# Optimization experiments

Measured on AMD Instinct MI355X. Metric: run time of the kernel, lower is better.

Reference implementation:

```python
import jax, jax.numpy as jnp
import numpy as np

E = 1024   # embed_dim
H = 16     # num_heads
D = E // H # head_dim
B = 2
S = 2048
YAT_EPS = 0.1


def setup_inputs() -> dict:
    key = jax.random.key(0)
    ks = jax.random.split(key, 5)
    w_scale = (6.0 / (E + E)) ** 0.5  # xavier_uniform bound
    def xavier(k):
        return jax.random.uniform(k, (E, E), jnp.float32, -w_scale, w_scale)
    return {
        "x": jax.random.normal(ks[0], (B, S, E), jnp.float32),
        "Wq": xavier(ks[1]), "bq": jnp.zeros((E,), jnp.float32),
        "Wk": xavier(ks[2]), "bk": jnp.zeros((E,), jnp.float32),
        "Wv": xavier(ks[3]), "bv": jnp.zeros((E,), jnp.float32),
        "Wo": xavier(ks[4]), "bo": jnp.zeros((E,), jnp.float32),
    }


def reference(x, Wq, bq, Wk, bk, Wv, bv, Wo, bo):
    b, s, _ = x.shape
    # Projections (Linear: x @ W + b, flax kernel layout [in, out])
    Q = x @ Wq + bq
    K = x @ Wk + bk
    V = x @ Wv + bv
    # [B, H, S, D]
    Q = Q.reshape(b, s, H, D).transpose(0, 2, 1, 3)
    K = K.reshape(b, s, H, D).transpose(0, 2, 1, 3)
    V = V.reshape(b, s, H, D).transpose(0, 2, 1, 3)
    # L2 normalize along head_dim
    Qn = Q / (jnp.linalg.norm(Q, axis=-1, keepdims=True) + 1e-8)
    Kn = K / (jnp.linalg.norm(K, axis=-1, keepdims=True) + 1e-8)
    # Yat kernel scores: (1 + <q,k>)^2 / (eps + (1 - <q,k>))
    dot = jnp.einsum("bhqd,bhkd->bhqk", Qn, Kn)
    scores = (1.0 + dot) ** 2 / (YAT_EPS + (1.0 - dot))
    # Sum-normalize (no softmax)
    attn = scores / (jnp.sum(scores, axis=-1, keepdims=True) + 1e-6)
    out = jnp.einsum("bhqk,bhkd->bhqd", attn, V)
    out = out.transpose(0, 2, 1, 3).reshape(b, s, E)
    return out @ Wo + bo
```

## Files before the change

kernel.cpp:

```cpp
#include <hip/hip_runtime.h>
#include <math.h>

#define EDIM 1024
#define NH   16
#define HD   64
#define BATCH 2
#define SEQ  2048
#define NROW (BATCH*SEQ)
#define YAT_EPS 0.1f

typedef _Float16 f16;
typedef _Float16 f16x8 __attribute__((ext_vector_type(8)));
typedef _Float16 f16x4 __attribute__((ext_vector_type(4)));
typedef __fp16   h16x2 __attribute__((ext_vector_type(2)));
typedef float    f32x4 __attribute__((ext_vector_type(4)));

static __device__ __forceinline__ int pk2(float a, float b) {
    union { h16x2 h; int i; } u;
    u.h = __builtin_amdgcn_cvt_pkrtz(a, b);
    return u.i;
}

__global__ __launch_bounds__(256)
void prep_kernel(const float* __restrict__ x, f16* __restrict__ xb,
                 const float* __restrict__ W0, const float* __restrict__ W1,
                 const float* __restrict__ W2, const float* __restrict__ W3,
                 f16* __restrict__ T0, f16* __restrict__ T1,
                 f16* __restrict__ T2, f16* __restrict__ T3)
{
    const int z = blockIdx.z;
    if (z == 4) {
        const int bid = blockIdx.y * 32 + blockIdx.x;
#pragma unroll
        for (int i = 0; i < 4; ++i) {
            const int off = bid * 4096 + i * 1024 + threadIdx.x * 4;
            const float4 v = *(const float4*)(x + off);
            union { int i2[2]; f16x4 h; } o;
            o.i2[0] = pk2(v.x, v.y);
            o.i2[1] = pk2(v.z, v.w);
            *(f16x4*)(xb + off) = o.h;
        }
        return;
    }
    const float* W = (z == 0) ? W0 : (z == 1) ? W1 : (z == 2) ? W2 : W3;
    f16*         Wt = (z == 0) ? T0 : (z == 1) ? T1 : (z == 2) ? T2 : T3;

    __shared__ float T[32][33];
    const int t = threadIdx.x;
    const int r = t >> 3, c4 = (t & 7) * 4;
    const int bi = blockIdx.x * 32, bj = blockIdx.y * 32;
    const float4 v = *(const float4*)(W + (size_t)(bi + r) * 1024 + bj + c4);
    T[r][c4 + 0] = v.x; T[r][c4 + 1] = v.y; T[r][c4 + 2] = v.z; T[r][c4 + 3] = v.w;
    __syncthreads();
    f16x4 o = {(f16)T[c4 + 0][r], (f16)T[c4 + 1][r], (f16)T[c4 + 2][r], (f16)T[c4 + 3][r]};
    *(f16x4*)(Wt + (size_t)(bj + r) * 1024 + bi + c4) = o;
}

template<int BM, int BN, int WM>
__global__ __launch_bounds__(WM * 128, 3)
void gemm_f16(const f16* __restrict__ A,
              const f16* __restrict__ B0, const f16* __restrict__ B1, const f16* __restrict__ B2,
              const float* __restrict__ bi0, const float* __restrict__ bi1, const float* __restrict__ bi2,
              void* __restrict__ o0, void* __restrict__ o1, void* __restrict__ o2,
              int e0, int e1, int e2)
{
    constexpr int NT    = WM * 128;
    constexpr int SR    = NT / 4;
    constexpr int ASL   = BM / SR;
    constexpr int BSL   = BN / SR;
    constexpr int ABUF  = BM * 32;
    constexpr int BBUF  = BN * 32;
    constexpr int WROWS = BM / WM;
    constexpr int MT    = WROWS / 16;
    constexpr int HALVES = BN / 128;
    constexpr int SCH    = 2048 / NT;
    __shared__ __align__(16) char lds[2 * (ABUF + BBUF) * 2];
    f16* As = (f16*)lds;
    f16* Bs = (f16*)lds + 2 * ABUF;

    const int z = blockIdx.z;
    const f16*   Bt   = (z == 0) ? B0  : (z == 1) ? B1  : B2;
    const float* bias = (z == 0) ? bi0 : (z == 1) ? bi1 : bi2;
    void*        Cout = (z == 0) ? o0  : (z == 1) ? o1  : o2;
    const int    epi  = (z == 0) ? e0  : (z == 1) ? e1  : e2;

    const int tid  = threadIdx.x;
    const int lane = tid & 63;
    const int w    = tid >> 6;
    const int cl   = lane & 15;
    const int quad = lane >> 4;
    const int wm = w % WM, wn = w / WM;
    const int bm = blockIdx.x * BM, bn = blockIdx.y * BN;
    const int wmoff = wm * WROWS;

    const int srow = tid >> 2;
    const int sc   = tid & 3;
    const int ssw  = (sc ^ (srow & 3)) * 8;
    const f16* gA = A  + (size_t)(bm + srow) * 1024 + sc * 8;
    const f16* gB = Bt + (size_t)(bn + srow) * 1024 + sc * 8;
    int lAo[ASL], lBo[BSL];
#pragma unroll
    for (int i = 0; i < ASL; ++i) lAo[i] = (srow + i * SR) * 32 + ssw;
#pragma unroll
    for (int i = 0; i < BSL; ++i) lBo[i] = (srow + i * SR) * 32 + ssw;

    f32x4 acc[MT][4];
#pragma unroll
    for (int i = 0; i < MT; ++i)
#pragma unroll
        for (int j = 0; j < 4; ++j) acc[i][j] = (f32x4){0.f, 0.f, 0.f, 0.f};

    f16x8 ra[ASL], rb[BSL];

#pragma unroll
    for (int i = 0; i < ASL; ++i) ra[i] = *(const f16x8*)(gA + (size_t)i * SR * 1024);
#pragma unroll
    for (int i = 0; i < BSL; ++i) rb[i] = *(const f16x8*)(gB + (size_t)i * SR * 1024);
#pragma unroll
    for (int i = 0; i < ASL; ++i) *(f16x8*)(As + lAo[i]) = ra[i];
#pragma unroll
    for (int i = 0; i < BSL; ++i) *(f16x8*)(Bs + lBo[i]) = rb[i];
#pragma unroll
    for (int i = 0; i < ASL; ++i) ra[i] = *(const f16x8*)(gA + (size_t)i * SR * 1024 + 32);
#pragma unroll
    for (int i = 0; i < BSL; ++i) rb[i] = *(const f16x8*)(gB + (size_t)i * SR * 1024 + 32);
    __syncthreads();

    const int fsw = (quad ^ (cl & 3)) * 8;

    for (int it = 0; it < 32; ++it) {
        const int buf = it & 1, nb = buf ^ 1;
        if (it < 31) {
#pragma unroll
            for (int i = 0; i < ASL; ++i) *(f16x8*)(As + nb * ABUF + lAo[i]) = ra[i];
#pragma unroll
            for (int i = 0; i < BSL; ++i) *(f16x8*)(Bs + nb * BBUF + lBo[i]) = rb[i];
        }
        if (it < 30) {
            const int kn = (it + 2) * 32;
#pragma unroll
            for (int i = 0; i < ASL; ++i) ra[i] = *(const f16x8*)(gA + (size_t)i * SR * 1024 + kn);
#pragma unroll
            for (int i = 0; i < BSL; ++i) rb[i] = *(const f16x8*)(gB + (size_t)i * SR * 1024 + kn);
        }
        f16x8 af[MT], bf[4];
#pragma unroll
        for (int mt = 0; mt < MT; ++mt)
            af[mt] = *(const f16x8*)(&As[buf * ABUF + (wmoff + mt * 16 + cl) * 32 + fsw]);
#pragma unroll
        for (int nt = 0; nt < 4; ++nt)
            bf[nt] = *(const f16x8*)(&Bs[buf * BBUF + (wn * 64 + nt * 16 + cl) * 32 + fsw]);
#pragma unroll
        for (int mt = 0; mt < MT; ++mt)
#pragma unroll
            for (int nt = 0; nt < 4; ++nt)
                acc[mt][nt] = __builtin_amdgcn_mfma_f32_16x16x32_f16(af[mt], bf[nt], acc[mt][nt], 0, 0, 0);
        __syncthreads();
    }

    float bcol[4];
#pragma unroll
    for (int nt = 0; nt < 4; ++nt) bcol[nt] = bias[bn + wn * 64 + nt * 16 + cl];
#pragma unroll
    for (int mt = 0; mt < MT; ++mt)
#pragma unroll
        for (int nt = 0; nt < 4; ++nt)
#pragma unroll
            for (int rg = 0; rg < 4; ++rg) acc[mt][nt][rg] += bcol[nt];

    const int b_idx = bm >> 11, sl0 = bm & (SEQ - 1), h0 = bn >> 6;

    if (epi == 0) {
        float* C = (float*)Cout;
#pragma unroll
        for (int mt = 0; mt < MT; ++mt)
#pragma unroll
            for (int rg = 0; rg < 4; ++rg) {
                const int row = bm + wmoff + mt * 16 + quad * 4 + rg;
#pragma unroll
                for (int nt = 0; nt < 4; ++nt)
                    C[(size_t)row * EDIM + bn + wn * 64 + nt * 16 + cl] = acc[mt][nt][rg];
            }
    } else if (epi == 1) {
        if constexpr (BM == 128) {
        f16* C = (f16*)Cout;
        f16* S = (f16*)lds;
#pragma unroll
        for (int h = 0; h < HALVES; ++h) {
            __syncthreads();
            if ((wn >> 1) == h) {
#pragma unroll
                for (int mt = 0; mt < MT; ++mt)
#pragma unroll
                    for (int rg = 0; rg < 4; ++rg) {
                        float ss = 0.f;
#pragma unroll
                        for (int nt = 0; nt < 4; ++nt) ss += acc[mt][nt][rg] * acc[mt][nt][rg];
                        ss += __shfl_xor(ss, 1); ss += __shfl_xor(ss, 2);
                        ss += __shfl_xor(ss, 4); ss += __shfl_xor(ss, 8);
                        const float inv = 1.0f / (sqrtf(ss) + 1e-8f);
                        const int row = wmoff + mt * 16 + quad * 4 + rg;
#pragma unroll
                        for (int nt = 0; nt < 4; ++nt) {
                            const int colh = (wn & 1) * 64 + nt * 16 + cl;
                            S[row * 128 + (((colh >> 3) ^ (row & 15)) * 8) + (colh & 7)] =
                                (f16)(acc[mt][nt][rg] * inv);
                        }
                    }
            }
            __syncthreads();
#pragma unroll
            for (int i = 0; i < SCH; ++i) {
                const int c = tid + i * NT;
                const int s = c >> 4, gi = c & 15;
                f16x8 v = *(const f16x8*)(&S[s * 128 + ((gi ^ (s & 15)) * 8)]);
                const int head = h0 + h * 2 + (gi >> 3), d8 = (gi & 7) * 8;
                *(f16x8*)(C + ((size_t)(b_idx * NH + head) * SEQ + sl0 + s) * HD + d8) = v;
            }
        }
        }
    } else {
        if constexpr (BM == 128) {
        f16* C = (f16*)Cout;
        f16* S = (f16*)lds;
#pragma unroll
        for (int h = 0; h < HALVES; ++h) {
            __syncthreads();
            if ((wn >> 1) == h) {
#pragma unroll
                for (int mt = 0; mt < MT; ++mt) {
                    const int s0 = wmoff + mt * 16 + quad * 4;
#pragma unroll
                    for (int nt = 0; nt < 4; ++nt) {
                        const int colh = (wn & 1) * 64 + nt * 16 + cl;
                        f16x4 o = {(f16)acc[mt][nt][0], (f16)acc[mt][nt][1],
                                   (f16)acc[mt][nt][2], (f16)acc[mt][nt][3]};
                        *(f16x4*)(&S[colh * 128 + (((s0 >> 3) ^ (colh & 15)) * 8) + (s0 & 7)]) = o;
                    }
                }
            }
            __syncthreads();
#pragma unroll
            for (int i = 0; i < SCH; ++i) {
                const int c = tid + i * NT;
                const int colh = c >> 4, gi = c & 15;
                f16x8 v = *(const f16x8*)(&S[colh * 128 + ((gi ^ (colh & 15)) * 8)]);
                const int head = h0 + h * 2 + (colh >> 6), d = colh & 63;
                *(f16x8*)(C + ((size_t)(b_idx * NH + head) * HD + d) * SEQ + sl0 + gi * 8) = v;
            }
        }
        }
    }
}

__global__ __launch_bounds__(256, 4)
void yat_attn(const f16* __restrict__ Qh, const f16* __restrict__ Kh,
              const f16* __restrict__ Vt, f16* __restrict__ AO)
{
    __shared__ __align__(16) char lds[40960];
    f16* Qs = (f16*)lds;
    f16* KB = (f16*)(lds + 8192);
    f16* VB = (f16*)(lds + 24576);

    const int tid  = threadIdx.x;
    const int lane = tid & 63;
    const int w    = tid >> 6;
    const int cl   = lane & 15;
    const int quad = lane >> 4;
    const int wm = w & 1;
    const int wk = w >> 1;
    const int q0 = blockIdx.x * 64;
    const int bh = blockIdx.y;

    const f16* Qg = Qh + (size_t)bh * SEQ * HD;
    const f16* Kg = Kh + (size_t)bh * SEQ * HD;
    const f16* Vg = Vt + (size_t)bh * HD * SEQ;

    const int r0 = tid >> 3;
    const int g0 = tid & 7;
    const f16* gK = Kg + (size_t)r0 * HD + g0 * 8;
    const f16* gV = Vg + (size_t)r0 * SEQ + g0 * 8;
    const int lkOff = r0 * 64 + ((g0 ^ (r0 & 7)) * 8);

    f16x8 kr0 = *(const f16x8*)(gK);
    f16x8 kr1 = *(const f16x8*)(gK + 32 * HD);
    f16x8 vr0 = *(const f16x8*)(gV);
    f16x8 vr1 = *(const f16x8*)(gV + (size_t)32 * SEQ);

#pragma unroll
    for (int i = 0; i < 2; ++i) {
        const int s0 = tid + i * 256;
        const int row = s0 >> 3, g = s0 & 7;
        f16x8 v = *(const f16x8*)(Qg + (size_t)(q0 + row) * HD + g * 8);
        *(f16x8*)(&Qs[row * 64 + ((g ^ (row & 7)) * 8)]) = v;
    }
    __syncthreads();
    f16x8 qf[2][2];
#pragma unroll
    for (int qt = 0; qt < 2; ++qt)
#pragma unroll
        for (int kb = 0; kb < 2; ++kb)
            qf[qt][kb] = *(const f16x8*)(&Qs[(wm * 32 + qt * 16 + cl) * 64 +
                                             ((kb * 4 + quad) ^ (cl & 7)) * 8]);

    f32x4 O[2][4];
    float rs[2] = {0.f, 0.f};
#pragma unroll
    for (int i = 0; i < 2; ++i)
#pragma unroll
        for (int j = 0; j < 4; ++j) O[i][j] = (f32x4){0.f, 0.f, 0.f, 0.f};

    for (int t = 0; t < 32; ++t) {
        const int buf = t & 1;
        *(f16x8*)(&KB[buf * 4096 + lkOff])        = kr0;
        *(f16x8*)(&KB[buf * 4096 + lkOff + 2048]) = kr1;
        *(f16x8*)(&VB[buf * 4096 + lkOff])        = vr0;
        *(f16x8*)(&VB[buf * 4096 + lkOff + 2048]) = vr1;
        if (t < 31) {
            kr0 = *(const f16x8*)(gK + (size_t)(t + 1) * 64 * HD);
            kr1 = *(const f16x8*)(gK + (size_t)(t + 1) * 64 * HD + 32 * HD);
            vr0 = *(const f16x8*)(gV + (t + 1) * 64);
            vr1 = *(const f16x8*)(gV + (size_t)32 * SEQ + (t + 1) * 64);
        }
        __syncthreads();

        const f16* Ks = KB + buf * 4096;
        const f16* Vs = VB + buf * 4096;

        f32x4 s[2][2];
#pragma unroll
        for (int kt = 0; kt < 2; ++kt)
#pragma unroll
            for (int qt = 0; qt < 2; ++qt) s[kt][qt] = (f32x4){0.f, 0.f, 0.f, 0.f};
#pragma unroll
        for (int kb = 0; kb < 2; ++kb) {
            const int sw = ((kb * 4 + quad) ^ (cl & 7)) * 8;
            f16x8 af0 = *(const f16x8*)(&Ks[(wk * 32 +  0 + cl) * 64 + sw]);
            f16x8 af1 = *(const f16x8*)(&Ks[(wk * 32 + 16 + cl) * 64 + sw]);
#pragma unroll
            for (int qt = 0; qt < 2; ++qt) {
                s[0][qt] = __builtin_amdgcn_mfma_f32_16x16x32_f16(af0, qf[qt][kb], s[0][qt], 0, 0, 0);
                s[1][qt] = __builtin_amdgcn_mfma_f32_16x16x32_f16(af1, qf[qt][kb], s[1][qt], 0, 0, 0);
            }
        }

        f16x4 pa16[2][2];
#pragma unroll
        for (int kt = 0; kt < 2; ++kt)
#pragma unroll
            for (int qt = 0; qt < 2; ++qt) {
                float p[4];
#pragma unroll
                for (int rg = 0; rg < 4; ++rg) {
                    const float u = (1.0f + YAT_EPS) - s[kt][qt][rg];
                    p[rg] = fmaf(4.41f, __builtin_amdgcn_rcpf(u), u - 4.2f);
                    rs[qt] += p[rg];
                }
                union { int i2[2]; f16x4 h; } pk_;
                pk_.i2[0] = pk2(p[0], p[1]);
                pk_.i2[1] = pk2(p[2], p[3]);
                pa16[kt][qt] = pk_.h;
            }

#pragma unroll
        for (int kt = 0; kt < 2; ++kt)
#pragma unroll
            for (int dn = 0; dn < 4; ++dn) {
                const int row = dn * 16 + cl;
                const int g = wk * 4 + kt * 2 + (quad >> 1);
                f16x4 vb = *(const f16x4*)(&Vs[row * 64 + ((g ^ (row & 7)) * 8) + (quad & 1) * 4]);
#pragma unroll
                for (int qt = 0; qt < 2; ++qt)
                    O[qt][dn] = __builtin_amdgcn_mfma_f32_16x16x16f16(pa16[kt][qt], vb, O[qt][dn], 0, 0, 0);
            }
    }

    __syncthreads();
    float* rs_s = (float*)lds;
    float* Ox   = (float*)(lds + 1024);

#pragma unroll
    for (int qt = 0; qt < 2; ++qt) {
        float t = rs[qt];
        t += __shfl_xor(t, 16);
        t += __shfl_xor(t, 32);
        if (quad == 0) rs_s[wk * 64 + wm * 32 + qt * 16 + cl] = t;
    }
    if (wk == 1) {
#pragma unroll
        for (int qt = 0; qt < 2; ++qt)
#pragma unroll
            for (int dn = 0; dn < 4; ++dn)
#pragma unroll
                for (int rg = 0; rg < 4; ++rg)
                    Ox[(wm * 32 + qt * 16 + quad * 4 + rg) * 64 + dn * 16 + cl] = O[qt][dn][rg];
    }
    __syncthreads();
    if (wk == 0) {
        const int b = bh >> 4, h = bh & 15;
#pragma unroll
        for (int qt = 0; qt < 2; ++qt)
#pragma unroll
            for (int rg = 0; rg < 4; ++rg) {
                const int ql = wm * 32 + qt * 16 + quad * 4 + rg;
                const float tot = rs_s[ql] + rs_s[64 + ql];
                const float inv = 1.0f / (tot + 1e-6f);
                const size_t rowoff = ((size_t)b * SEQ + q0 + ql) * EDIM + h * 64;
#pragma unroll
                for (int dn = 0; dn < 4; ++dn)
                    AO[rowoff + dn * 16 + cl] =
                        (f16)((O[qt][dn][rg] + Ox[ql * 64 + dn * 16 + cl]) * inv);
            }
    }
}

extern "C" void kernel_launch(void* const* d_in, const int* in_sizes, int n_in,
                              void* d_out, int out_size, void* d_ws, size_t ws_size,
                              hipStream_t stream)
{
    const float* x  = (const float*)d_in[0];
    const float* Wq = (const float*)d_in[1];
    const float* bq = (const float*)d_in[2];
    const float* Wk = (const float*)d_in[3];
    const float* bk = (const float*)d_in[4];
    const float* Wv = (const float*)d_in[5];
    const float* bv = (const float*)d_in[6];
    const float* Wo = (const float*)d_in[7];
    const float* bo = (const float*)d_in[8];

    char* p = (char*)d_ws;
    f16* xb  = (f16*)p;                 p += (size_t)NROW * EDIM * 2;
    f16* Wqt = (f16*)p;                 p += (size_t)EDIM * EDIM * 2;
    f16* Wkt = (f16*)p;                 p += (size_t)EDIM * EDIM * 2;
    f16* Wvt = (f16*)p;                 p += (size_t)EDIM * EDIM * 2;
    f16* Wot = (f16*)p;                 p += (size_t)EDIM * EDIM * 2;
    f16* Qhb = (f16*)p;                 p += (size_t)NROW * EDIM * 2;
    f16* Khb = (f16*)p;                 p += (size_t)NROW * EDIM * 2;
    f16* Vtb = (f16*)p;                 p += (size_t)NROW * EDIM * 2;
    f16* AOb = (f16*)p;                 p += (size_t)NROW * EDIM * 2;

    prep_kernel<<<dim3(32, 32, 5), 256, 0, stream>>>(x, xb, Wq, Wk, Wv, Wo,
                                                     Wqt, Wkt, Wvt, Wot);

    gemm_f16<128, 128, 4><<<dim3(NROW / 128, EDIM / 128, 3), 512, 0, stream>>>(
        xb, Wqt, Wkt, Wvt, bq, bk, bv, Qhb, Khb, Vtb, 1, 1, 2);

    yat_attn<<<dim3(SEQ / 64, BATCH * NH), 256, 0, stream>>>(Qhb, Khb, Vtb, AOb);

    gemm_f16<64, 128, 2><<<dim3(NROW / 64, EDIM / 128, 1), 256, 0, stream>>>(
        AOb, Wot, Wot, Wot, bo, bo, bo, d_out, d_out, d_out, 0, 0, 0);
}
```

Baseline: 201.3 us.

## Enlarge attention tiles to 128 queries and 128 keys with 512 threads

New measurement: 226.7 us. +12.6%, slower.

```diff
diff --git a/kernel.cpp b/kernel.cpp
--- a/kernel.cpp
+++ b/kernel.cpp
@@ -253,55 +253,49 @@
     }
 }
 
-__global__ __launch_bounds__(256, 4)
+__global__ __launch_bounds__(512, 4)
 void yat_attn(const f16* __restrict__ Qh, const f16* __restrict__ Kh,
               const f16* __restrict__ Vt, f16* __restrict__ AO)
 {
-    __shared__ __align__(16) char lds[40960];
-    f16* Qs = (f16*)lds;
-    f16* KB = (f16*)(lds + 8192);
-    f16* VB = (f16*)(lds + 24576);
+    __shared__ __align__(16) char lds[65536];
+    f16* KB = (f16*)lds;
+    f16* VB = (f16*)(lds + 32768);
 
     const int tid  = threadIdx.x;
     const int lane = tid & 63;
     const int w    = tid >> 6;
     const int cl   = lane & 15;
     const int quad = lane >> 4;
-    const int wm = w & 1;
-    const int wk = w >> 1;
-    const int q0 = blockIdx.x * 64;
+    const int wm = w & 3;
+    const int wk = w >> 2;
+    const int q0 = blockIdx.x * 128;
     const int bh = blockIdx.y;
 
     const f16* Qg = Qh + (size_t)bh * SEQ * HD;
     const f16* Kg = Kh + (size_t)bh * SEQ * HD;
     const f16* Vg = Vt + (size_t)bh * HD * SEQ;
 
-    const int r0 = tid >> 3;
-    const int g0 = tid & 7;
-    const f16* gK = Kg + (size_t)r0 * HD + g0 * 8;
-    const f16* gV = Vg + (size_t)r0 * SEQ + g0 * 8;
-    const int lkOff = r0 * 64 + ((g0 ^ (r0 & 7)) * 8);
+    const int rk = tid >> 3;
+    const int gk = tid & 7;
+    const f16* gK = Kg + (size_t)rk * HD + gk * 8;
+    const int kOff = rk * 64 + ((gk ^ (rk & 7)) * 8);
+    const int rv = tid >> 4;
+    const int gv = tid & 15;
+    const f16* gV = Vg + (size_t)rv * SEQ + gv * 8;
+    const int vOff = rv * 128 + ((gv ^ (rv & 15)) * 8);
 
     f16x8 kr0 = *(const f16x8*)(gK);
-    f16x8 kr1 = *(const f16x8*)(gK + 32 * HD);
+    f16x8 kr1 = *(const f16x8*)(gK + 64 * HD);
     f16x8 vr0 = *(const f16x8*)(gV);
     f16x8 vr1 = *(const f16x8*)(gV + (size_t)32 * SEQ);
 
-#pragma unroll
-    for (int i = 0; i < 2; ++i) {
-        const int s0 = tid + i * 256;
-        const int row = s0 >> 3, g = s0 & 7;
-        f16x8 v = *(const f16x8*)(Qg + (size_t)(q0 + row) * HD + g * 8);
-        *(f16x8*)(&Qs[row * 64 + ((g ^ (row & 7)) * 8)]) = v;
-    }
-    __syncthreads();
     f16x8 qf[2][2];
 #pragma unroll
     for (int qt = 0; qt < 2; ++qt)
 #pragma unroll
         for (int kb = 0; kb < 2; ++kb)
-            qf[qt][kb] = *(const f16x8*)(&Qs[(wm * 32 + qt * 16 + cl) * 64 +
-                                             ((kb * 4 + quad) ^ (cl & 7)) * 8]);
+            qf[qt][kb] = *(const f16x8*)(Qg + (size_t)(q0 + wm * 32 + qt * 16 + cl) * HD +
+                                         (kb * 4 + quad) * 8);
 
     f32x4 O[2][4];
     float rs[2] = {0.f, 0.f};
@@ -310,72 +304,71 @@
 #pragma unroll
         for (int j = 0; j < 4; ++j) O[i][j] = (f32x4){0.f, 0.f, 0.f, 0.f};
 
-    for (int t = 0; t < 32; ++t) {
+    for (int t = 0; t < 16; ++t) {
         const int buf = t & 1;
-        *(f16x8*)(&KB[buf * 4096 + lkOff])        = kr0;
-        *(f16x8*)(&KB[buf * 4096 + lkOff + 2048]) = kr1;
-        *(f16x8*)(&VB[buf * 4096 + lkOff])        = vr0;
-        *(f16x8*)(&VB[buf * 4096 + lkOff + 2048]) = vr1;
-        if (t < 31) {
-            kr0 = *(const f16x8*)(gK + (size_t)(t + 1) * 64 * HD);
-            kr1 = *(const f16x8*)(gK + (size_t)(t + 1) * 64 * HD + 32 * HD);
-            vr0 = *(const f16x8*)(gV + (t + 1) * 64);
-            vr1 = *(const f16x8*)(gV + (size_t)32 * SEQ + (t + 1) * 64);
+        f16* Ks = KB + buf * 8192;
+        f16* Vs = VB + buf * 8192;
+        *(f16x8*)(Ks + kOff)        = kr0;
+        *(f16x8*)(Ks + kOff + 4096) = kr1;
+        *(f16x8*)(Vs + vOff)        = vr0;
+        *(f16x8*)(Vs + vOff + 4096) = vr1;
+        if (t < 15) {
+            const f16* nK = gK + (size_t)(t + 1) * 128 * HD;
+            const f16* nV = gV + (t + 1) * 128;
+            kr0 = *(const f16x8*)(nK);
+            kr1 = *(const f16x8*)(nK + 64 * HD);
+            vr0 = *(const f16x8*)(nV);
+            vr1 = *(const f16x8*)(nV + (size_t)32 * SEQ);
         }
         __syncthreads();
 
-        const f16* Ks = KB + buf * 4096;
-        const f16* Vs = VB + buf * 4096;
-
-        f32x4 s[2][2];
-#pragma unroll
-        for (int kt = 0; kt < 2; ++kt)
-#pragma unroll
-            for (int qt = 0; qt < 2; ++qt) s[kt][qt] = (f32x4){0.f, 0.f, 0.f, 0.f};
-#pragma unroll
-        for (int kb = 0; kb < 2; ++kb) {
-            const int sw = ((kb * 4 + quad) ^ (cl & 7)) * 8;
-            f16x8 af0 = *(const f16x8*)(&Ks[(wk * 32 +  0 + cl) * 64 + sw]);
-            f16x8 af1 = *(const f16x8*)(&Ks[(wk * 32 + 16 + cl) * 64 + sw]);
-#pragma unroll
-            for (int qt = 0; qt < 2; ++qt) {
-                s[0][qt] = __builtin_amdgcn_mfma_f32_16x16x32_f16(af0, qf[qt][kb], s[0][qt], 0, 0, 0);
-                s[1][qt] = __builtin_amdgcn_mfma_f32_16x16x32_f16(af1, qf[qt][kb], s[1][qt], 0, 0, 0);
-            }
-        }
-
-        f16x4 pa16[2][2];
-#pragma unroll
-        for (int kt = 0; kt < 2; ++kt)
-#pragma unroll
-            for (int qt = 0; qt < 2; ++qt) {
-                float p[4];
+#pragma unroll
+        for (int kt = 0; kt < 4; ++kt) {
+            const int krow = (wk * 64 + kt * 16 + cl) * 64;
+            f16x8 a0 = *(const f16x8*)(&Ks[krow + ((quad     ^ (cl & 7)) * 8)]);
+            f16x8 a1 = *(const f16x8*)(&Ks[krow + (((4 + quad) ^ (cl & 7)) * 8)]);
+            f32x4 s0 = (f32x4){0.f, 0.f, 0.f, 0.f};
+            f32x4 s1 = (f32x4){0.f, 0.f, 0.f, 0.f};
+            __builtin_amdgcn_s_setprio(1);
+            s0 = __builtin_amdgcn_mfma_f32_16x16x32_f16(a0, qf[0][0], s0, 0, 0, 0);
+            s0 = __builtin_amdgcn_mfma_f32_16x16x32_f16(a1, qf[0][1], s0, 0, 0, 0);
+            s1 = __builtin_amdgcn_mfma_f32_16x16x32_f16(a0, qf[1][0], s1, 0, 0, 0);
+            s1 = __builtin_amdgcn_mfma_f32_16x16x32_f16(a1, qf[1][1], s1, 0, 0, 0);
+            __builtin_amdgcn_s_setprio(0);
+
+            f16x4 pa0, pa1;
+            {
+                float p0[4], p1[4];
 #pragma unroll
                 for (int rg = 0; rg < 4; ++rg) {
-                    const float u = (1.0f + YAT_EPS) - s[kt][qt][rg];
-                    p[rg] = fmaf(4.41f, __builtin_amdgcn_rcpf(u), u - 4.2f);
-                    rs[qt] += p[rg];
+                    const float u0 = (1.0f + YAT_EPS) - s0[rg];
+                    const float u1 = (1.0f + YAT_EPS) - s1[rg];
+                    p0[rg] = fmaf(4.41f, __builtin_amdgcn_rcpf(u0), u0 - 4.2f);
+                    p1[rg] = fmaf(4.41f, __builtin_amdgcn_rcpf(u1), u1 - 4.2f);
+                    rs[0] += p0[rg];
+                    rs[1] += p1[rg];
                 }
                 union { int i2[2]; f16x4 h; } pk_;
-                pk_.i2[0] = pk2(p[0], p[1]);
-                pk_.i2[1] = pk2(p[2], p[3]);
-                pa16[kt][qt] = pk_.h;
-            }
-
-#pragma unroll
-        for (int kt = 0; kt < 2; ++kt)
+                pk_.i2[0] = pk2(p0[0], p0[1]); pk_.i2[1] = pk2(p0[2], p0[3]);
+                pa0 = pk_.h;
+                pk_.i2[0] = pk2(p1[0], p1[1]); pk_.i2[1] = pk2(p1[2], p1[3]);
+                pa1 = pk_.h;
+            }
+
+            const int g = wk * 8 + kt * 2 + (quad >> 1);
+            __builtin_amdgcn_s_setprio(1);
 #pragma unroll
             for (int dn = 0; dn < 4; ++dn) {
                 const int row = dn * 16 + cl;
-                const int g = wk * 4 + kt * 2 + (quad >> 1);
-                f16x4 vb = *(const f16x4*)(&Vs[row * 64 + ((g ^ (row & 7)) * 8) + (quad & 1) * 4]);
-#pragma unroll
-                for (int qt = 0; qt < 2; ++qt)
-                    O[qt][dn] = __builtin_amdgcn_mfma_f32_16x16x16f16(pa16[kt][qt], vb, O[qt][dn], 0, 0, 0);
-            }
-    }
-
-    __syncthreads();
+                f16x4 vb = *(const f16x4*)(&Vs[row * 128 + ((g ^ (row & 15)) * 8) + (quad & 1) * 4]);
+                O[0][dn] = __builtin_amdgcn_mfma_f32_16x16x16f16(pa0, vb, O[0][dn], 0, 0, 0);
+                O[1][dn] = __builtin_amdgcn_mfma_f32_16x16x16f16(pa1, vb, O[1][dn], 0, 0, 0);
+            }
+            __builtin_amdgcn_s_setprio(0);
+        }
+        __syncthreads();
+    }
+
     float* rs_s = (float*)lds;
     float* Ox   = (float*)(lds + 1024);
 
@@ -384,7 +377,7 @@
         float t = rs[qt];
         t += __shfl_xor(t, 16);
         t += __shfl_xor(t, 32);
-        if (quad == 0) rs_s[wk * 64 + wm * 32 + qt * 16 + cl] = t;
+        if (quad == 0) rs_s[wk * 128 + wm * 32 + qt * 16 + cl] = t;
     }
     if (wk == 1) {
 #pragma unroll
@@ -403,7 +396,7 @@
 #pragma unroll
             for (int rg = 0; rg < 4; ++rg) {
                 const int ql = wm * 32 + qt * 16 + quad * 4 + rg;
-                const float tot = rs_s[ql] + rs_s[64 + ql];
+                const float tot = rs_s[ql] + rs_s[128 + ql];
                 const float inv = 1.0f / (tot + 1e-6f);
                 const size_t rowoff = ((size_t)b * SEQ + q0 + ql) * EDIM + h * 64;
 #pragma unroll
@@ -445,7 +438,7 @@
     gemm_f16<128, 128, 4><<<dim3(NROW / 128, EDIM / 128, 3), 512, 0, stream>>>(
         xb, Wqt, Wkt, Wvt, bq, bk, bv, Qhb, Khb, Vtb, 1, 1, 2);
 
-    yat_attn<<<dim3(SEQ / 64, BATCH * NH), 256, 0, stream>>>(Qhb, Khb, Vtb, AOb);
+    yat_attn<<<dim3(SEQ / 128, BATCH * NH), 512, 0, stream>>>(Qhb, Khb, Vtb, AOb);
 
     gemm_f16<64, 128, 2><<<dim3(NROW / 64, EDIM / 128, 1), 256, 0, stream>>>(
         AOb, Wot, Wot, Wot, bo, bo, bo, d_out, d_out, d_out, 0, 0, 0);
```

## Enlarge Yat attention tile to 128 queries with 8 waves, packed-f32 math and setprio

Applied to the files above, without the earlier changes.

After: 199.3 us. About the same (-1.0%).

```diff
diff --git a/kernel.cpp b/kernel.cpp
--- a/kernel.cpp
+++ b/kernel.cpp
@@ -14,11 +14,23 @@
 typedef _Float16 f16x4 __attribute__((ext_vector_type(4)));
 typedef __fp16   h16x2 __attribute__((ext_vector_type(2)));
 typedef float    f32x4 __attribute__((ext_vector_type(4)));
+typedef float    f32x2 __attribute__((ext_vector_type(2)));
 
 static __device__ __forceinline__ int pk2(float a, float b) {
     union { h16x2 h; int i; } u;
     u.h = __builtin_amdgcn_cvt_pkrtz(a, b);
     return u.i;
+}
+
+static __device__ __forceinline__ f32x2 pk_fma(f32x2 a, f32x2 b, f32x2 c) {
+    f32x2 d;
+    asm("v_pk_fma_f32 %0, %1, %2, %3" : "=v"(d) : "v"(a), "v"(b), "v"(c));
+    return d;
+}
+static __device__ __forceinline__ f32x2 pk_add(f32x2 a, f32x2 b) {
+    f32x2 d;
+    asm("v_pk_add_f32 %0, %1, %2" : "=v"(d) : "v"(a), "v"(b));
+    return d;
 }
 
 __global__ __launch_bounds__(256)
@@ -253,43 +265,41 @@
     }
 }
 
-__global__ __launch_bounds__(256, 4)
+__global__ __launch_bounds__(512, 4)
 void yat_attn(const f16* __restrict__ Qh, const f16* __restrict__ Kh,
               const f16* __restrict__ Vt, f16* __restrict__ AO)
 {
-    __shared__ __align__(16) char lds[40960];
+    __shared__ __align__(16) char lds[49152];
     f16* Qs = (f16*)lds;
-    f16* KB = (f16*)(lds + 8192);
-    f16* VB = (f16*)(lds + 24576);
+    f16* KB = (f16*)(lds + 16384);
+    f16* VB = (f16*)(lds + 32768);
 
     const int tid  = threadIdx.x;
     const int lane = tid & 63;
     const int w    = tid >> 6;
     const int cl   = lane & 15;
     const int quad = lane >> 4;
-    const int wm = w & 1;
-    const int wk = w >> 1;
-    const int q0 = blockIdx.x * 64;
+    const int wm = w & 3;
+    const int wk = w >> 2;
+    const int q0 = blockIdx.x * 128;
     const int bh = blockIdx.y;
 
     const f16* Qg = Qh + (size_t)bh * SEQ * HD;
     const f16* Kg = Kh + (size_t)bh * SEQ * HD;
     const f16* Vg = Vt + (size_t)bh * HD * SEQ;
 
-    const int r0 = tid >> 3;
-    const int g0 = tid & 7;
-    const f16* gK = Kg + (size_t)r0 * HD + g0 * 8;
-    const f16* gV = Vg + (size_t)r0 * SEQ + g0 * 8;
-    const int lkOff = r0 * 64 + ((g0 ^ (r0 & 7)) * 8);
-
-    f16x8 kr0 = *(const f16x8*)(gK);
-    f16x8 kr1 = *(const f16x8*)(gK + 32 * HD);
-    f16x8 vr0 = *(const f16x8*)(gV);
-    f16x8 vr1 = *(const f16x8*)(gV + (size_t)32 * SEQ);
+    const int rkv = tid >> 3;
+    const int gkv = tid & 7;
+    const f16* gK = Kg + (size_t)rkv * HD + gkv * 8;
+    const f16* gV = Vg + (size_t)rkv * SEQ + gkv * 8;
+    const int lkOff = rkv * 64 + ((gkv ^ (rkv & 7)) * 8);
+
+    f16x8 kr = *(const f16x8*)(gK);
+    f16x8 vr = *(const f16x8*)(gV);
 
 #pragma unroll
     for (int i = 0; i < 2; ++i) {
-        const int s0 = tid + i * 256;
+        const int s0 = tid + i * 512;
         const int row = s0 >> 3, g = s0 & 7;
         f16x8 v = *(const f16x8*)(Qg + (size_t)(q0 + row) * HD + g * 8);
         *(f16x8*)(&Qs[row * 64 + ((g ^ (row & 7)) * 8)]) = v;
@@ -304,23 +314,26 @@
                                              ((kb * 4 + quad) ^ (cl & 7)) * 8]);
 
     f32x4 O[2][4];
-    float rs[2] = {0.f, 0.f};
-#pragma unroll
-    for (int i = 0; i < 2; ++i)
+    f32x2 rs_pk[2];
+#pragma unroll
+    for (int i = 0; i < 2; ++i) {
+        rs_pk[i] = (f32x2){0.f, 0.f};
 #pragma unroll
         for (int j = 0; j < 4; ++j) O[i][j] = (f32x4){0.f, 0.f, 0.f, 0.f};
+    }
+
+    const f32x2 c_m1  = {-1.0f, -1.0f};
+    const f32x2 c_u0  = {1.0f + YAT_EPS, 1.0f + YAT_EPS};
+    const f32x2 c_m42 = {-4.2f, -4.2f};
+    const f32x2 c_441 = {4.41f, 4.41f};
 
     for (int t = 0; t < 32; ++t) {
         const int buf = t & 1;
-        *(f16x8*)(&KB[buf * 4096 + lkOff])        = kr0;
-        *(f16x8*)(&KB[buf * 4096 + lkOff + 2048]) = kr1;
-        *(f16x8*)(&VB[buf * 4096 + lkOff])        = vr0;
-        *(f16x8*)(&VB[buf * 4096 + lkOff + 2048]) = vr1;
+        *(f16x8*)(&KB[buf * 4096 + lkOff]) = kr;
+        *(f16x8*)(&VB[buf * 4096 + lkOff]) = vr;
         if (t < 31) {
-            kr0 = *(const f16x8*)(gK + (size_t)(t + 1) * 64 * HD);
-            kr1 = *(const f16x8*)(gK + (size_t)(t + 1) * 64 * HD + 32 * HD);
-            vr0 = *(const f16x8*)(gV + (t + 1) * 64);
-            vr1 = *(const f16x8*)(gV + (size_t)32 * SEQ + (t + 1) * 64);
+            kr = *(const f16x8*)(gK + (size_t)(t + 1) * 64 * HD);
+            vr = *(const f16x8*)(gV + (t + 1) * 64);
         }
         __syncthreads();
 
@@ -332,6 +345,7 @@
         for (int kt = 0; kt < 2; ++kt)
 #pragma unroll
             for (int qt = 0; qt < 2; ++qt) s[kt][qt] = (f32x4){0.f, 0.f, 0.f, 0.f};
+        __builtin_amdgcn_s_setprio(1);
 #pragma unroll
         for (int kb = 0; kb < 2; ++kb) {
             const int sw = ((kb * 4 + quad) ^ (cl & 7)) * 8;
@@ -343,25 +357,30 @@
                 s[1][qt] = __builtin_amdgcn_mfma_f32_16x16x32_f16(af1, qf[qt][kb], s[1][qt], 0, 0, 0);
             }
         }
+        __builtin_amdgcn_s_setprio(0);
 
         f16x4 pa16[2][2];
 #pragma unroll
         for (int kt = 0; kt < 2; ++kt)
 #pragma unroll
             for (int qt = 0; qt < 2; ++qt) {
-                float p[4];
-#pragma unroll
-                for (int rg = 0; rg < 4; ++rg) {
-                    const float u = (1.0f + YAT_EPS) - s[kt][qt][rg];
-                    p[rg] = fmaf(4.41f, __builtin_amdgcn_rcpf(u), u - 4.2f);
-                    rs[qt] += p[rg];
-                }
+                f32x2 d01 = {s[kt][qt][0], s[kt][qt][1]};
+                f32x2 d23 = {s[kt][qt][2], s[kt][qt][3]};
+                f32x2 u01 = pk_fma(d01, c_m1, c_u0);
+                f32x2 u23 = pk_fma(d23, c_m1, c_u0);
+                f32x2 r01 = {__builtin_amdgcn_rcpf(u01[0]), __builtin_amdgcn_rcpf(u01[1])};
+                f32x2 r23 = {__builtin_amdgcn_rcpf(u23[0]), __builtin_amdgcn_rcpf(u23[1])};
+                f32x2 p01 = pk_fma(c_441, r01, pk_add(u01, c_m42));
+                f32x2 p23 = pk_fma(c_441, r23, pk_add(u23, c_m42));
+                rs_pk[qt] = pk_add(rs_pk[qt], p01);
+                rs_pk[qt] = pk_add(rs_pk[qt], p23);
                 union { int i2[2]; f16x4 h; } pk_;
-                pk_.i2[0] = pk2(p[0], p[1]);
-                pk_.i2[1] = pk2(p[2], p[3]);
+                pk_.i2[0] = pk2(p01[0], p01[1]);
+                pk_.i2[1] = pk2(p23[0], p23[1]);
                 pa16[kt][qt] = pk_.h;
             }
 
+        __builtin_amdgcn_s_setprio(1);
 #pragma unroll
         for (int kt = 0; kt < 2; ++kt)
 #pragma unroll
@@ -373,6 +392,7 @@
                 for (int qt = 0; qt < 2; ++qt)
                     O[qt][dn] = __builtin_amdgcn_mfma_f32_16x16x16f16(pa16[kt][qt], vb, O[qt][dn], 0, 0, 0);
             }
+        __builtin_amdgcn_s_setprio(0);
     }
 
     __syncthreads();
@@ -381,10 +401,10 @@
 
 #pragma unroll
     for (int qt = 0; qt < 2; ++qt) {
-        float t = rs[qt];
+        float t = rs_pk[qt][0] + rs_pk[qt][1];
         t += __shfl_xor(t, 16);
         t += __shfl_xor(t, 32);
-        if (quad == 0) rs_s[wk * 64 + wm * 32 + qt * 16 + cl] = t;
+        if (quad == 0) rs_s[wk * 128 + wm * 32 + qt * 16 + cl] = t;
     }
     if (wk == 1) {
 #pragma unroll
@@ -403,7 +423,7 @@
 #pragma unroll
             for (int rg = 0; rg < 4; ++rg) {
                 const int ql = wm * 32 + qt * 16 + quad * 4 + rg;
-                const float tot = rs_s[ql] + rs_s[64 + ql];
+                const float tot = rs_s[ql] + rs_s[128 + ql];
                 const float inv = 1.0f / (tot + 1e-6f);
                 const size_t rowoff = ((size_t)b * SEQ + q0 + ql) * EDIM + h * 64;
 #pragma unroll
@@ -445,7 +465,7 @@
     gemm_f16<128, 128, 4><<<dim3(NROW / 128, EDIM / 128, 3), 512, 0, stream>>>(
         xb, Wqt, Wkt, Wvt, bq, bk, bv, Qhb, Khb, Vtb, 1, 1, 2);
 
-    yat_attn<<<dim3(SEQ / 64, BATCH * NH), 256, 0, stream>>>(Qhb, Khb, Vtb, AOb);
+    yat_attn<<<dim3(SEQ / 128, BATCH * NH), 512, 0, stream>>>(Qhb, Khb, Vtb, AOb);
 
     gemm_f16<64, 128, 2><<<dim3(NROW / 64, EDIM / 128, 1), 256, 0, stream>>>(
         AOb, Wot, Wot, Wot, bo, bo, bo, d_out, d_out, d_out, 0, 0, 0);
```
